# Kernel optimization log

Measured on AMD Instinct MI355X. Metric: run time of the kernel, lower is better.

The kernel has to match this reference:

```python
import jax, jax.numpy as jnp
import numpy as np
from jax import lax

N_HEAD, D_IN, D_HID, D_OUT = 8, 64, 64, 64
SEQ = 32768
STD = 1.0 / np.sqrt(D_HID * N_HEAD)


def _unif(key, shape):
    return jax.random.uniform(key, shape, jnp.float32, -STD, STD)


def setup_inputs() -> dict:
    key = jax.random.key(0)
    ks = jax.random.split(key, 12)
    D = N_HEAD * D_IN
    return {
        "inputs": jax.random.normal(ks[0], (SEQ, D), jnp.float32),
        "W_in": _unif(ks[1], (D, D)),
        "b_in": _unif(ks[2], (D,)),
        "W_gates": _unif(ks[3], (D_IN, 3 * D_HID)),
        "b_gates": _unif(ks[4], (3 * D_HID,)),
        "W_og": _unif(ks[5], (D_IN, D_HID)),
        "b_og": _unif(ks[6], (D_HID,)),
        "W_c": _unif(ks[7], (D_HID, D_OUT)),
        "b_c": _unif(ks[8], (D_OUT,)),
        "W_out": _unif(ks[9], (N_HEAD * D_OUT, N_HEAD * D_OUT)),
        "b_out": _unif(ks[10], (N_HEAD * D_OUT,)),
    }


def reference(inputs, W_in, b_in, W_gates, b_gates, W_og, b_og, W_c, b_c, W_out, b_out):
    S = inputs.shape[0]
    # input mixing across heads, then flatten: (S, H*d_in) -> (S*H, d_in)
    x = (inputs @ W_in + b_in).reshape(S * N_HEAD, D_IN)
    # FirstModule: fused gate projection
    g = x @ W_gates + b_gates  # (S*H, 3*d_hid)
    fg = jax.nn.sigmoid(g[:, :D_HID])
    ig = jax.nn.sigmoid(g[:, D_HID:2 * D_HID])
    h = jnp.tanh(g[:, 2 * D_HID:])
    hr = ig * h
    # linear recurrence c_t = fg_t * c_{t-1} + hr_t, c_0 = 0, via associative scan
    def comb(e1, e2):
        a1, b1 = e1
        a2, b2 = e2
        return (a1 * a2, b1 * a2 + b2)
    _, c = lax.associative_scan(comb, (fg, hr))  # (S*H, d_hid)
    # SecondModule: output gate and projection
    og = jax.nn.sigmoid(x @ W_og + b_og)
    o = (og * c) @ W_c + b_c  # (S*H, d_out)
    o = o.reshape(S, N_HEAD * D_OUT)
    return o @ W_out + b_out
```

## Files before the change

kernel.cpp:

```cpp
#include <hip/hip_runtime.h>


typedef unsigned short ushort;
typedef __bf16 bf16x8 __attribute__((ext_vector_type(8)));
typedef float f32x4 __attribute__((ext_vector_type(4)));

#define CROWS 64
#define NCH  4096
#define NSUP 64

#define GLOAD16(gp, lp) __builtin_amdgcn_global_load_lds( \
    (const __attribute__((address_space(1))) void*)(gp),  \
    (__attribute__((address_space(3))) void*)(lp), 16, 0, 0)

__device__ inline float b2f(ushort u) {
    return __builtin_bit_cast(float, (unsigned)u << 16);
}
__device__ inline ushort f2b(float f) {
    unsigned x = __builtin_bit_cast(unsigned, f);
    x += 0x7FFFu + ((x >> 16) & 1u);
    return (ushort)(x >> 16);
}
__device__ inline float sigm(float v) { return __builtin_amdgcn_rcpf(1.0f + __expf(-v)); }
__device__ inline float tanh_fast(float v) {
    return 2.0f * __builtin_amdgcn_rcpf(1.0f + __expf(-2.0f * v)) - 1.0f;
}
__device__ inline f32x4 MFMA(bf16x8 a, bf16x8 b, f32x4 c) {
    return __builtin_amdgcn_mfma_f32_16x16x32_bf16(a, b, c, 0, 0, 0);
}

__global__ void transpose512(const float* __restrict__ src, ushort* __restrict__ dst) {
    __shared__ float tile[32][33];
    const int tx = threadIdx.x & 31, ty = threadIdx.x >> 5;
    const int x0 = blockIdx.x * 32, y0 = blockIdx.y * 32;
    #pragma unroll
    for (int dy = 0; dy < 32; dy += 8)
        tile[ty + dy][tx] = src[(size_t)(y0 + ty + dy) * 512 + x0 + tx];
    __syncthreads();
    #pragma unroll
    for (int dy = 0; dy < 32; dy += 8)
        dst[(size_t)(x0 + ty + dy) * 512 + y0 + tx] = f2b(tile[tx][ty + dy]);
}

__global__ void prep_small(const float* __restrict__ W_gates, const float* __restrict__ W_og,
                           const float* __restrict__ W_c,
                           const float* __restrict__ b_gates, const float* __restrict__ b_og,
                           ushort* __restrict__ W2T, ushort* __restrict__ WcT, float* __restrict__ b2) {
    const int idx = blockIdx.x * 256 + threadIdx.x;
    if (idx < 16384) {
        const int n = idx >> 6, k = idx & 63;
        float v;
        if      (n < 64)  v = W_gates[k * 192 + 64 + n];
        else if (n < 128) v = W_gates[k * 192 + 128 + (n - 64)];
        else if (n < 192) v = W_gates[k * 192 + (n - 128)];
        else              v = W_og[k * 64 + (n - 192)];
        W2T[idx] = f2b(v);
    } else if (idx < 16384 + 4096) {
        const int i = idx - 16384;
        const int n = i >> 6, k = i & 63;
        WcT[i] = f2b(W_c[(k << 6) + n]);
    } else if (idx < 16384 + 4096 + 256) {
        const int i = idx - 20480;
        float v;
        if      (i < 64)  v = b_gates[64 + i];
        else if (i < 128) v = b_gates[128 + (i - 64)];
        else if (i < 192) v = b_gates[i - 128];
        else              v = b_og[i - 192];
        b2[i] = v;
    }
}

__global__ __launch_bounds__(256)
void cvt_f32_bf16(const float* __restrict__ src, ushort* __restrict__ dst) {
    const long i = ((long)blockIdx.x * 256 + threadIdx.x) * 8;
    const float4 v0 = *(const float4*)(src + i);
    const float4 v1 = *(const float4*)(src + i + 4);
    *(ushort4*)(dst + i)     = make_ushort4(f2b(v0.x), f2b(v0.y), f2b(v0.z), f2b(v0.w));
    *(ushort4*)(dst + i + 4) = make_ushort4(f2b(v1.x), f2b(v1.y), f2b(v1.z), f2b(v1.w));
}

template <int BM, int BN, int WAVES_M, int WAVES_N, int A32, int C32>
__global__ __launch_bounds__(256)
void gemm_bt(const void* __restrict__ Av, const ushort* __restrict__ Bt,
             const float* __restrict__ bias, void* __restrict__ Cv,
             int M, int N, int K) {
    constexpr int WM = BM / WAVES_M, WN = BN / WAVES_N;
    constexpr int MT = WM / 16, NT = WN / 16;
    __shared__ __align__(16) ushort sA[BM * 32];
    __shared__ __align__(16) ushort sB[BN * 32];

    const int t = threadIdx.x, w = t >> 6, lane = t & 63;
    const int wm = (w / WAVES_N) * WM, wn = (w % WAVES_N) * WN;
    const long bm = (long)blockIdx.x * BM, bn = (long)blockIdx.y * BN;

    f32x4 acc[MT][NT] = {};

    for (int k0 = 0; k0 < K; k0 += 32) {
        if (A32) {
            const float* A = (const float*)Av;
            #pragma unroll
            for (int is = 0; is < BM / 32; ++is) {
                const int row = is * 32 + (t >> 3);
                const int cd = (t & 7) >> 1, half = t & 1;
                const float4 v = *(const float4*)(A + (bm + row) * (long)K + k0 + (t & 7) * 4);
                *(ushort4*)&sA[row * 32 + ((cd ^ (row & 3)) * 8) + half * 4] =
                    make_ushort4(f2b(v.x), f2b(v.y), f2b(v.z), f2b(v.w));
            }
        } else {
            const ushort* A = (const ushort*)Av;
            #pragma unroll
            for (int is = 0; is < BM / 64; ++is) {
                const int row = t >> 2, kc = t & 3;
                GLOAD16(A + (bm + is * 64 + row) * (long)K + k0 + ((kc ^ (row & 3)) * 8),
                        (char*)sA + is * 4096 + w * 1024);
            }
        }
        #pragma unroll
        for (int is = 0; is < BN / 64; ++is) {
            const int row = t >> 2, kc = t & 3;
            GLOAD16(Bt + (bn + is * 64 + row) * (long)K + k0 + ((kc ^ (row & 3)) * 8),
                    (char*)sB + is * 4096 + w * 1024);
        }
        __syncthreads();

        bf16x8 af[MT], bfr[NT];
        #pragma unroll
        for (int i = 0; i < MT; ++i) {
            const int row = wm + i * 16 + (lane & 15), c = lane >> 4;
            af[i] = *(const bf16x8*)&sA[row * 32 + ((c ^ (row & 3)) * 8)];
        }
        #pragma unroll
        for (int j = 0; j < NT; ++j) {
            const int rb = wn + j * 16 + (lane & 15), c = lane >> 4;
            bfr[j] = *(const bf16x8*)&sB[rb * 32 + ((c ^ (rb & 3)) * 8)];
        }
        #pragma unroll
        for (int i = 0; i < MT; ++i)
            #pragma unroll
            for (int j = 0; j < NT; ++j)
                acc[i][j] = MFMA(af[i], bfr[j], acc[i][j]);
        __syncthreads();
    }

    #pragma unroll
    for (int i = 0; i < MT; ++i)
        #pragma unroll
        for (int j = 0; j < NT; ++j) {
            const long col = bn + wn + j * 16 + (lane & 15);
            const float bv = bias[col];
            #pragma unroll
            for (int r = 0; r < 4; ++r) {
                const long row = bm + wm + i * 16 + ((lane >> 4) << 2) + r;
                const float v = acc[i][j][r] + bv;
                if (C32) ((float*)Cv)[row * (long)N + col] = v;
                else     ((ushort*)Cv)[row * (long)N + col] = f2b(v);
            }
        }
}

template <int APPLY>
__global__ __launch_bounds__(256, 4)
void gates_scan(const ushort* __restrict__ X, const ushort* __restrict__ W2T,
                const float* __restrict__ b2, const ushort* __restrict__ WcT,
                const float* __restrict__ b_c,
                float* __restrict__ Agg, float* __restrict__ Bgg,
                const float* __restrict__ PreS, ushort* __restrict__ O) {
    __shared__ __align__(16) char smem[APPLY ? 35840 : 18432];
    ushort* sFG = (ushort*)smem;
    ushort* sHR = (ushort*)(smem + 9216);
    ushort* sOG = (ushort*)(smem + 18432);
    ushort* sP  = (ushort*)(smem + 27648);

    const int t = threadIdx.x, w = t >> 6, lane = t & 63;
    const int blk = blockIdx.x;
    const long row0 = (long)blk * CROWS;

    const int wm = (w >> 1) * 32;
    const int grpB = w & 1;
    const int colbase = grpB * 128;
    const int lr = lane & 15, lc = lane >> 4;

    bf16x8 af[2][2];
    #pragma unroll
    for (int kk = 0; kk < 2; ++kk)
        #pragma unroll
        for (int i = 0; i < 2; ++i)
            af[kk][i] = *(const bf16x8*)(X + (row0 + wm + i * 16 + lr) * 64 + kk * 32 + lc * 8);

    f32x4 acc[2][8] = {};
    #pragma unroll
    for (int kk = 0; kk < 2; ++kk)
        #pragma unroll
        for (int j = 0; j < 8; ++j) {
            const bf16x8 bf = *(const bf16x8*)(W2T + (colbase + j * 16 + lr) * 64 + kk * 32 + lc * 8);
            acc[0][j] = MFMA(af[kk][0], bf, acc[0][j]);
            acc[1][j] = MFMA(af[kk][1], bf, acc[1][j]);
        }

    if (!grpB) {
        #pragma unroll
        for (int jj = 0; jj < 4; ++jj) {
            const int ch = jj * 16 + lr;
            const float bi = b2[ch], bh = b2[64 + ch];
            #pragma unroll
            for (int i = 0; i < 2; ++i)
                #pragma unroll
                for (int r = 0; r < 4; ++r) {
                    const int row = wm + i * 16 + (lc << 2) + r;
                    const float gi = acc[i][jj][r] + bi;
                    const float gh = acc[i][jj + 4][r] + bh;
                    sHR[row * 72 + ch] = f2b(sigm(gi) * tanh_fast(gh));
                }
        }
    } else {
        #pragma unroll
        for (int jj = 0; jj < 4; ++jj) {
            const int ch = jj * 16 + lr;
            const float bfg = b2[128 + ch], bog = b2[192 + ch];
            #pragma unroll
            for (int i = 0; i < 2; ++i)
                #pragma unroll
                for (int r = 0; r < 4; ++r) {
                    const int row = wm + i * 16 + (lc << 2) + r;
                    sFG[row * 72 + ch] = f2b(sigm(acc[i][jj][r] + bfg));
                    if (APPLY) sOG[row * 72 + ch] = f2b(sigm(acc[i][jj + 4][r] + bog));
                }
        }
    }
    __syncthreads();

    if (!APPLY) {
        if (t < 64) {
            float a = 1.0f, b = 0.0f;
            #pragma unroll 8
            for (int r = 0; r < CROWS; ++r) {
                const float fg = b2f(sFG[r * 72 + t]);
                const float hr = b2f(sHR[r * 72 + t]);
                a *= fg;
                b = fmaf(b, fg, hr);
            }
            Agg[blk * 64 + t] = a;
            Bgg[blk * 64 + t] = b;
        }
        return;
    }

    if (t < 64) {
        float c = fmaf(PreS[(blk >> 6) * 64 + t], Agg[blk * 64 + t], Bgg[blk * 64 + t]);
        const int cch = t >> 3, half = t & 7;
        #pragma unroll 8
        for (int r = 0; r < CROWS; ++r) {
            const float fg = b2f(sFG[r * 72 + t]);
            const float hr = b2f(sHR[r * 72 + t]);
            c = fmaf(c, fg, hr);
            sP[r * 64 + ((cch ^ (r & 7)) * 8) + half] = f2b(b2f(sOG[r * 72 + t]) * c);
        }
    }
    __syncthreads();

    const int wn2 = grpB * 32;
    f32x4 acc2[2][2] = {};
    #pragma unroll
    for (int kk = 0; kk < 2; ++kk) {
        bf16x8 pa[2], wb[2];
        #pragma unroll
        for (int i = 0; i < 2; ++i) {
            const int row = wm + i * 16 + lr, c = kk * 4 + lc;
            pa[i] = *(const bf16x8*)&sP[row * 64 + ((c ^ (row & 7)) * 8)];
        }
        #pragma unroll
        for (int j = 0; j < 2; ++j)
            wb[j] = *(const bf16x8*)(WcT + (wn2 + j * 16 + lr) * 64 + kk * 32 + lc * 8);
        #pragma unroll
        for (int i = 0; i < 2; ++i)
            #pragma unroll
            for (int j = 0; j < 2; ++j)
                acc2[i][j] = MFMA(pa[i], wb[j], acc2[i][j]);
    }
    #pragma unroll
    for (int i = 0; i < 2; ++i)
        #pragma unroll
        for (int j = 0; j < 2; ++j) {
            const int col = wn2 + j * 16 + lr;
            const float bv = b_c[col];
            #pragma unroll
            for (int r = 0; r < 4; ++r) {
                const int row = wm + i * 16 + (lc << 2) + r;
                O[(row0 + row) * 64 + col] = f2b(acc2[i][j][r] + bv);
            }
        }
}

__global__ void scan_super(float* __restrict__ Agg, float* __restrict__ Bgg,
                           float* __restrict__ SA, float* __restrict__ SB) {
    const int s = blockIdx.x, ch = threadIdx.x;
    float a = 1.0f, b = 0.0f;
    #pragma unroll 8
    for (int j = 0; j < 64; ++j) {
        const int idx = (s * 64 + j) * 64 + ch;
        const float a2 = Agg[idx], bb = Bgg[idx];
        Agg[idx] = a;
        Bgg[idx] = b;
        a *= a2;
        b = fmaf(b, a2, bb);
    }
    SA[s * 64 + ch] = a;
    SB[s * 64 + ch] = b;
}

__global__ void scan_top(const float* __restrict__ SA, const float* __restrict__ SB,
                         float* __restrict__ PreS) {
    const int ch = threadIdx.x;
    float c = 0.0f;
    #pragma unroll 8
    for (int s = 0; s < 64; ++s) {
        PreS[s * 64 + ch] = c;
        c = fmaf(c, SA[s * 64 + ch], SB[s * 64 + ch]);
    }
}

extern "C" void kernel_launch(void* const* d_in, const int* in_sizes, int n_in,
                              void* d_out, int out_size, void* d_ws, size_t ws_size,
                              hipStream_t stream) {
    const float* inputs  = (const float*)d_in[0];
    const float* W_in    = (const float*)d_in[1];
    const float* b_in    = (const float*)d_in[2];
    const float* W_gates = (const float*)d_in[3];
    const float* b_gates = (const float*)d_in[4];
    const float* W_og    = (const float*)d_in[5];
    const float* b_og    = (const float*)d_in[6];
    const float* W_c     = (const float*)d_in[7];
    const float* b_c     = (const float*)d_in[8];
    const float* W_out   = (const float*)d_in[9];
    const float* b_out   = (const float*)d_in[10];
    float* out = (float*)d_out;

    char* ws = (char*)d_ws;
    ushort* X     = (ushort*)(ws);
    ushort* WinT  = (ushort*)(ws + 33554432);
    ushort* WoutT = (ushort*)(ws + 34078720);
    ushort* W2T   = (ushort*)(ws + 34603008);
    ushort* WcT   = (ushort*)(ws + 34635776);
    float*  b2    = (float*)(ws + 34643968);
    float*  Agg   = (float*)(ws + 34644992);
    float*  Bgg   = (float*)(ws + 35693568);
    float*  SA    = (float*)(ws + 36742144);
    float*  SB    = (float*)(ws + 36758528);
    float*  PreS  = (float*)(ws + 36774912);
    ushort* Ibf   = (ushort*)(ws + 36791296);
    ushort* O = X;
    const bool big_ws = ws_size >= (36791296ull + 33554432ull);

    transpose512<<<dim3(16, 16), 256, 0, stream>>>(W_in, WinT);
    transpose512<<<dim3(16, 16), 256, 0, stream>>>(W_out, WoutT);
    prep_small<<<81, 256, 0, stream>>>(W_gates, W_og, W_c, b_gates, b_og, W2T, WcT, b2);

    if (big_ws) {
        cvt_f32_bf16<<<8192, 256, 0, stream>>>(inputs, Ibf);
        gemm_bt<128, 128, 2, 2, 0, 0><<<dim3(256, 4), 256, 0, stream>>>(
            Ibf, WinT, b_in, X, 32768, 512, 512);
    } else {
        gemm_bt<128, 128, 2, 2, 1, 0><<<dim3(256, 4), 256, 0, stream>>>(
            inputs, WinT, b_in, X, 32768, 512, 512);
    }

    gates_scan<0><<<NCH, 256, 0, stream>>>(X, W2T, b2, WcT, b_c, Agg, Bgg, PreS, O);
    scan_super<<<NSUP, 64, 0, stream>>>(Agg, Bgg, SA, SB);
    scan_top<<<1, 64, 0, stream>>>(SA, SB, PreS);
    gates_scan<1><<<NCH, 256, 0, stream>>>(X, W2T, b2, WcT, b_c, Agg, Bgg, PreS, O);

    gemm_bt<128, 128, 2, 2, 0, 1><<<dim3(256, 4), 256, 0, stream>>>(
        O, WoutT, b_out, out, 32768, 512, 512);
}
```

Before: 317.2 us.

## Store gate activations in first pass to avoid recomputing GEMM in apply pass

Adds a gates_store kernel that computes the gate projection once, writes packed bf16 forget/hr pairs and the output gate to global memory, and emits per-chunk scan aggregates. A new scan_apply kernel rereads those stored values instead of reloading X and recomputing the gate MFMA and transcendentals, then applies the prefix and the W_c projection. This trades recomputation for extra global traffic (about 12 bytes per element written and read back) and uses d_out as scratch for the output gate. The new path runs only when the workspace is large enough.

New measurement: 288.6 us. -9.0%, faster.

```diff
diff --git a/kernel.cpp b/kernel.cpp
--- a/kernel.cpp
+++ b/kernel.cpp
@@ -158,6 +158,192 @@
         }
 }
 
+__global__ __launch_bounds__(256, 4)
+void gates_store(const ushort* __restrict__ X, const ushort* __restrict__ W2T,
+                 const float* __restrict__ b2,
+                 unsigned* __restrict__ FGHR, ushort* __restrict__ OGg,
+                 float* __restrict__ Agg, float* __restrict__ Bgg) {
+    __shared__ __align__(16) char smem[29696];
+    ushort* sFG = (ushort*)smem;
+    ushort* sHR = (ushort*)(smem + 9216);
+    ushort* sOG = (ushort*)(smem + 18432);
+    float*  spa = (float*)(smem + 27648);
+    float*  spb = (float*)(smem + 28672);
+
+    const int t = threadIdx.x, w = t >> 6, lane = t & 63;
+    const int blk = blockIdx.x;
+    const long row0 = (long)blk * CROWS;
+
+    const int wm = (w >> 1) * 32;
+    const int grpB = w & 1;
+    const int colbase = grpB * 128;
+    const int lr = lane & 15, lc = lane >> 4;
+
+    bf16x8 af[2][2];
+    #pragma unroll
+    for (int kk = 0; kk < 2; ++kk)
+        #pragma unroll
+        for (int i = 0; i < 2; ++i)
+            af[kk][i] = *(const bf16x8*)(X + (row0 + wm + i * 16 + lr) * 64 + kk * 32 + lc * 8);
+
+    f32x4 acc[2][8] = {};
+    #pragma unroll
+    for (int kk = 0; kk < 2; ++kk)
+        #pragma unroll
+        for (int j = 0; j < 8; ++j) {
+            const bf16x8 bf = *(const bf16x8*)(W2T + (colbase + j * 16 + lr) * 64 + kk * 32 + lc * 8);
+            acc[0][j] = MFMA(af[kk][0], bf, acc[0][j]);
+            acc[1][j] = MFMA(af[kk][1], bf, acc[1][j]);
+        }
+
+    if (!grpB) {
+        #pragma unroll
+        for (int jj = 0; jj < 4; ++jj) {
+            const int ch = jj * 16 + lr;
+            const float bi = b2[ch], bh = b2[64 + ch];
+            #pragma unroll
+            for (int i = 0; i < 2; ++i)
+                #pragma unroll
+                for (int r = 0; r < 4; ++r) {
+                    const int row = wm + i * 16 + (lc << 2) + r;
+                    const float gi = acc[i][jj][r] + bi;
+                    const float gh = acc[i][jj + 4][r] + bh;
+                    sHR[row * 72 + ch] = f2b(sigm(gi) * tanh_fast(gh));
+                }
+        }
+    } else {
+        #pragma unroll
+        for (int jj = 0; jj < 4; ++jj) {
+            const int ch = jj * 16 + lr;
+            const float bfg = b2[128 + ch], bog = b2[192 + ch];
+            #pragma unroll
+            for (int i = 0; i < 2; ++i)
+                #pragma unroll
+                for (int r = 0; r < 4; ++r) {
+                    const int row = wm + i * 16 + (lc << 2) + r;
+                    sFG[row * 72 + ch] = f2b(sigm(acc[i][jj][r] + bfg));
+                    sOG[row * 72 + ch] = f2b(sigm(acc[i][jj + 4][r] + bog));
+                }
+        }
+    }
+    __syncthreads();
+
+    {
+        const int ch = lane;
+        float a = 1.0f, b = 0.0f;
+        #pragma unroll
+        for (int r = 0; r < 16; ++r) {
+            const int row = (w << 4) + r;
+            const ushort ufg = sFG[row * 72 + ch];
+            const ushort uhr = sHR[row * 72 + ch];
+            FGHR[(row0 + row) * 64 + ch] = (unsigned)ufg | ((unsigned)uhr << 16);
+            OGg[(row0 + row) * 64 + ch] = sOG[row * 72 + ch];
+            const float fg = b2f(ufg), hr = b2f(uhr);
+            a *= fg;
+            b = fmaf(b, fg, hr);
+        }
+        spa[(w << 6) + ch] = a;
+        spb[(w << 6) + ch] = b;
+    }
+    __syncthreads();
+
+    if (t < 64) {
+        float a = spa[t], b = spb[t];
+        #pragma unroll
+        for (int k = 1; k < 4; ++k) {
+            const float a2 = spa[(k << 6) + t];
+            const float bb = spb[(k << 6) + t];
+            a *= a2;
+            b = fmaf(b, a2, bb);
+        }
+        Agg[blk * 64 + t] = a;
+        Bgg[blk * 64 + t] = b;
+    }
+}
+
+__global__ __launch_bounds__(256, 4)
+void scan_apply(const unsigned* __restrict__ FGHR, const ushort* __restrict__ OGg,
+                const float* __restrict__ Agg, const float* __restrict__ Bgg,
+                const float* __restrict__ PreS,
+                const ushort* __restrict__ WcT, const float* __restrict__ b_c,
+                ushort* __restrict__ O) {
+    __shared__ __align__(16) char smem[10240];
+    ushort* sP  = (ushort*)smem;
+    float*  spa = (float*)(smem + 8192);
+    float*  spb = (float*)(smem + 9216);
+
+    const int t = threadIdx.x, w = t >> 6, lane = t & 63;
+    const int blk = blockIdx.x;
+    const long row0 = (long)blk * CROWS;
+    const int ch = lane;
+
+    unsigned fh[16];
+    {
+        float a = 1.0f, b = 0.0f;
+        #pragma unroll
+        for (int r = 0; r < 16; ++r) {
+            fh[r] = FGHR[(row0 + (w << 4) + r) * 64 + ch];
+            const float fg = b2f((ushort)fh[r]);
+            const float hr = b2f((ushort)(fh[r] >> 16));
+            a *= fg;
+            b = fmaf(b, fg, hr);
+        }
+        spa[(w << 6) + ch] = a;
+        spb[(w << 6) + ch] = b;
+    }
+    __syncthreads();
+
+    float c = fmaf(PreS[(blk >> 6) * 64 + ch], Agg[blk * 64 + ch], Bgg[blk * 64 + ch]);
+    for (int k = 0; k < w; ++k)
+        c = fmaf(c, spa[(k << 6) + ch], spb[(k << 6) + ch]);
+
+    const int cch = ch >> 3, half = ch & 7;
+    #pragma unroll
+    for (int r = 0; r < 16; ++r) {
+        const int row = (w << 4) + r;
+        const float fg = b2f((ushort)fh[r]);
+        const float hr = b2f((ushort)(fh[r] >> 16));
+        c = fmaf(c, fg, hr);
+        const float og = b2f(OGg[(row0 + row) * 64 + ch]);
+        sP[row * 64 + ((cch ^ (row & 7)) * 8) + half] = f2b(og * c);
+    }
+    __syncthreads();
+
+    const int wm = (w >> 1) * 32;
+    const int wn2 = (w & 1) * 32;
+    const int lr = lane & 15, lc = lane >> 4;
+    f32x4 acc2[2][2] = {};
+    #pragma unroll
+    for (int kk = 0; kk < 2; ++kk) {
+        bf16x8 pa[2], wb[2];
+        #pragma unroll
+        for (int i = 0; i < 2; ++i) {
+            const int row = wm + i * 16 + lr, cidx = kk * 4 + lc;
+            pa[i] = *(const bf16x8*)&sP[row * 64 + ((cidx ^ (row & 7)) * 8)];
+        }
+        #pragma unroll
+        for (int j = 0; j < 2; ++j)
+            wb[j] = *(const bf16x8*)(WcT + (wn2 + j * 16 + lr) * 64 + kk * 32 + lc * 8);
+        #pragma unroll
+        for (int i = 0; i < 2; ++i)
+            #pragma unroll
+            for (int j = 0; j < 2; ++j)
+                acc2[i][j] = MFMA(pa[i], wb[j], acc2[i][j]);
+    }
+    #pragma unroll
+    for (int i = 0; i < 2; ++i)
+        #pragma unroll
+        for (int j = 0; j < 2; ++j) {
+            const int col = wn2 + j * 16 + lr;
+            const float bv = b_c[col];
+            #pragma unroll
+            for (int r = 0; r < 4; ++r) {
+                const int row = wm + i * 16 + (lc << 2) + r;
+                O[(row0 + row) * 64 + col] = f2b(acc2[i][j][r] + bv);
+            }
+        }
+}
+
 template <int APPLY>
 __global__ __launch_bounds__(256, 4)
 void gates_scan(const ushort* __restrict__ X, const ushort* __restrict__ W2T,
@@ -348,26 +534,41 @@
     float*  SB    = (float*)(ws + 36758528);
     float*  PreS  = (float*)(ws + 36774912);
     ushort* Ibf   = (ushort*)(ws + 36791296);
+    unsigned* FGHR = (unsigned*)(ws + 36791296);
+    ushort* OGg   = (ushort*)d_out;
     ushort* O = X;
-    const bool big_ws = ws_size >= (36791296ull + 33554432ull);
+
+    const bool new_path = ws_size >= 103900160ull;
+    const bool big_ws   = ws_size >= 70345728ull;
 
     transpose512<<<dim3(16, 16), 256, 0, stream>>>(W_in, WinT);
     transpose512<<<dim3(16, 16), 256, 0, stream>>>(W_out, WoutT);
     prep_small<<<81, 256, 0, stream>>>(W_gates, W_og, W_c, b_gates, b_og, W2T, WcT, b2);
 
-    if (big_ws) {
+    if (new_path) {
         cvt_f32_bf16<<<8192, 256, 0, stream>>>(inputs, Ibf);
         gemm_bt<128, 128, 2, 2, 0, 0><<<dim3(256, 4), 256, 0, stream>>>(
             Ibf, WinT, b_in, X, 32768, 512, 512);
+        gates_store<<<NCH, 256, 0, stream>>>(X, W2T, b2, FGHR, OGg, Agg, Bgg);
+        scan_super<<<NSUP, 64, 0, stream>>>(Agg, Bgg, SA, SB);
+        scan_top<<<1, 64, 0, stream>>>(SA, SB, PreS);
+        scan_apply<<<NCH, 256, 0, stream>>>(FGHR, OGg, Agg, Bgg, PreS, WcT, b_c, O);
+    } else if (big_ws) {
+        cvt_f32_bf16<<<8192, 256, 0, stream>>>(inputs, Ibf);
+        gemm_bt<128, 128, 2, 2, 0, 0><<<dim3(256, 4), 256, 0, stream>>>(
+            Ibf, WinT, b_in, X, 32768, 512, 512);
+        gates_scan<0><<<NCH, 256, 0, stream>>>(X, W2T, b2, WcT, b_c, Agg, Bgg, PreS, O);
+        scan_super<<<NSUP, 64, 0, stream>>>(Agg, Bgg, SA, SB);
+        scan_top<<<1, 64, 0, stream>>>(SA, SB, PreS);
+        gates_scan<1><<<NCH, 256, 0, stream>>>(X, W2T, b2, WcT, b_c, Agg, Bgg, PreS, O);
     } else {
         gemm_bt<128, 128, 2, 2, 1, 0><<<dim3(256, 4), 256, 0, stream>>>(
             inputs, WinT, b_in, X, 32768, 512, 512);
-    }
-
-    gates_scan<0><<<NCH, 256, 0, stream>>>(X, W2T, b2, WcT, b_c, Agg, Bgg, PreS, O);
-    scan_super<<<NSUP, 64, 0, stream>>>(Agg, Bgg, SA, SB);
-    scan_top<<<1, 64, 0, stream>>>(SA, SB, PreS);
-    gates_scan<1><<<NCH, 256, 0, stream>>>(X, W2T, b2, WcT, b_c, Agg, Bgg, PreS, O);
+        gates_scan<0><<<NCH, 256, 0, stream>>>(X, W2T, b2, WcT, b_c, Agg, Bgg, PreS, O);
+        scan_super<<<NSUP, 64, 0, stream>>>(Agg, Bgg, SA, SB);
+        scan_top<<<1, 64, 0, stream>>>(SA, SB, PreS);
+        gates_scan<1><<<NCH, 256, 0, stream>>>(X, W2T, b2, WcT, b_c, Agg, Bgg, PreS, O);
+    }
 
     gemm_bt<128, 128, 2, 2, 0, 1><<<dim3(256, 4), 256, 0, stream>>>(
         O, WoutT, b_out, out, 32768, 512, 512);
```

## Give each wavefront its own 64-row chunk in gate/scan kernels

Applied to the files above, without the earlier changes.

Adds gates_agg and scan_apply kernels, used on the large-workspace path, in which each wavefront owns a whole 64-row chunk. It computes gate projections with MFMA in 16-row sub-tiles, stages packed forget/input values in per-wave LDS and runs the per-channel recurrence with all 64 lanes, one channel per lane. The old kernels left three of four waves idle during the serial scan and synchronised the whole block. The new layout drops block-wide barriers and makes all lanes scan, at the cost of reloading weights from global memory per wave and using smaller MFMA tiles. The Wc projection is folded into the same per-wave loop.

New measurement: 348.4 us. 1.1x slower.

```diff
diff --git a/kernel.cpp b/kernel.cpp
--- a/kernel.cpp
+++ b/kernel.cpp
@@ -158,6 +158,148 @@
         }
 }
 
+__global__ __launch_bounds__(256, 4)
+void gates_agg(const ushort* __restrict__ X, const ushort* __restrict__ W2T,
+               const float* __restrict__ b2,
+               float* __restrict__ Agg, float* __restrict__ Bgg) {
+    __shared__ __align__(16) unsigned sW[4][16 * 64];
+
+    const int t = threadIdx.x, w = t >> 6, lane = t & 63;
+    const int lr = lane & 15, lc = lane >> 4;
+    const long chunk = (long)blockIdx.x * 4 + w;
+    const long row0 = chunk * 64;
+
+    float a = 1.0f, b = 0.0f;
+    #pragma unroll 1
+    for (int bt = 0; bt < 4; ++bt) {
+        const long rb = row0 + bt * 16;
+        const bf16x8 af0 = *(const bf16x8*)(X + (rb + lr) * 64 + lc * 8);
+        const bf16x8 af1 = *(const bf16x8*)(X + (rb + lr) * 64 + 32 + lc * 8);
+
+        #pragma unroll
+        for (int g = 0; g < 4; ++g) {
+            f32x4 aig = {}, ah = {}, afg = {};
+            #pragma unroll
+            for (int kk = 0; kk < 2; ++kk) {
+                const bf16x8 w0 = *(const bf16x8*)(W2T + (g * 16 + lr) * 64 + kk * 32 + lc * 8);
+                const bf16x8 w1 = *(const bf16x8*)(W2T + (64 + g * 16 + lr) * 64 + kk * 32 + lc * 8);
+                const bf16x8 w2 = *(const bf16x8*)(W2T + (128 + g * 16 + lr) * 64 + kk * 32 + lc * 8);
+                const bf16x8 afk = kk ? af1 : af0;
+                aig = MFMA(afk, w0, aig);
+                ah  = MFMA(afk, w1, ah);
+                afg = MFMA(afk, w2, afg);
+            }
+            const int ch = g * 16 + lr;
+            const float bi = b2[ch], bh = b2[64 + ch], bfg = b2[128 + ch];
+            #pragma unroll
+            for (int r = 0; r < 4; ++r) {
+                const int row = (lc << 2) + r;
+                const float hr = sigm(aig[r] + bi) * tanh_fast(ah[r] + bh);
+                const float fg = sigm(afg[r] + bfg);
+                sW[w][row * 64 + (ch ^ (lc << 4))] =
+                    (unsigned)f2b(fg) | ((unsigned)f2b(hr) << 16);
+            }
+        }
+        #pragma unroll
+        for (int r = 0; r < 16; ++r) {
+            const unsigned fh = sW[w][r * 64 + (lane ^ ((r >> 2) << 4))];
+            const float fg = b2f((ushort)fh);
+            const float hr = b2f((ushort)(fh >> 16));
+            a *= fg;
+            b = fmaf(b, fg, hr);
+        }
+    }
+    Agg[chunk * 64 + lane] = a;
+    Bgg[chunk * 64 + lane] = b;
+}
+
+__global__ __launch_bounds__(256, 4)
+void scan_apply(const ushort* __restrict__ X, const ushort* __restrict__ W2T,
+                const float* __restrict__ b2,
+                const float* __restrict__ Agg, const float* __restrict__ Bgg,
+                const float* __restrict__ PreS,
+                const ushort* __restrict__ WcT, const float* __restrict__ b_c,
+                ushort* __restrict__ O) {
+    __shared__ __align__(16) unsigned sW[4][16 * 64];
+    __shared__ __align__(16) ushort  sOG[4][16 * 64];
+    __shared__ __align__(16) ushort  sP [4][16 * 64];
+
+    const int t = threadIdx.x, w = t >> 6, lane = t & 63;
+    const int lr = lane & 15, lc = lane >> 4;
+    const long chunk = (long)blockIdx.x * 4 + w;
+    const long row0 = chunk * 64;
+
+    float c = fmaf(PreS[(chunk >> 6) * 64 + lane], Agg[chunk * 64 + lane],
+                   Bgg[chunk * 64 + lane]);
+
+    const int cch = lane >> 3, half = lane & 7;
+
+    #pragma unroll 1
+    for (int bt = 0; bt < 4; ++bt) {
+        const long rb = row0 + bt * 16;
+        const bf16x8 af0 = *(const bf16x8*)(X + (rb + lr) * 64 + lc * 8);
+        const bf16x8 af1 = *(const bf16x8*)(X + (rb + lr) * 64 + 32 + lc * 8);
+
+        #pragma unroll
+        for (int g = 0; g < 4; ++g) {
+            f32x4 aig = {}, ah = {}, afg = {}, aog = {};
+            #pragma unroll
+            for (int kk = 0; kk < 2; ++kk) {
+                const bf16x8 w0 = *(const bf16x8*)(W2T + (g * 16 + lr) * 64 + kk * 32 + lc * 8);
+                const bf16x8 w1 = *(const bf16x8*)(W2T + (64 + g * 16 + lr) * 64 + kk * 32 + lc * 8);
+                const bf16x8 w2 = *(const bf16x8*)(W2T + (128 + g * 16 + lr) * 64 + kk * 32 + lc * 8);
+                const bf16x8 w3 = *(const bf16x8*)(W2T + (192 + g * 16 + lr) * 64 + kk * 32 + lc * 8);
+                const bf16x8 afk = kk ? af1 : af0;
+                aig = MFMA(afk, w0, aig);
+                ah  = MFMA(afk, w1, ah);
+                afg = MFMA(afk, w2, afg);
+                aog = MFMA(afk, w3, aog);
+            }
+            const int ch = g * 16 + lr;
+            const float bi = b2[ch], bh = b2[64 + ch];
+            const float bfg = b2[128 + ch], bog = b2[192 + ch];
+            #pragma unroll
+            for (int r = 0; r < 4; ++r) {
+                const int row = (lc << 2) + r;
+                const float hr = sigm(aig[r] + bi) * tanh_fast(ah[r] + bh);
+                const float fg = sigm(afg[r] + bfg);
+                const int sl = row * 64 + (ch ^ (lc << 4));
+                sW[w][sl]  = (unsigned)f2b(fg) | ((unsigned)f2b(hr) << 16);
+                sOG[w][sl] = f2b(sigm(aog[r] + bog));
+            }
+        }
+
+        #pragma unroll
+        for (int r = 0; r < 16; ++r) {
+            const int sl = r * 64 + (lane ^ ((r >> 2) << 4));
+            const unsigned fh = sW[w][sl];
+            const float og = b2f(sOG[w][sl]);
+            c = fmaf(c, b2f((ushort)fh), b2f((ushort)(fh >> 16)));
+            sP[w][r * 64 + ((cch ^ (r & 7)) * 8) + half] = f2b(og * c);
+        }
+
+        f32x4 acc2[4] = {};
+        #pragma unroll
+        for (int kk = 0; kk < 2; ++kk) {
+            const int cidx = kk * 4 + lc;
+            const bf16x8 pa = *(const bf16x8*)&sP[w][lr * 64 + ((cidx ^ (lr & 7)) * 8)];
+            #pragma unroll
+            for (int j = 0; j < 4; ++j) {
+                const bf16x8 wc = *(const bf16x8*)(WcT + (j * 16 + lr) * 64 + kk * 32 + lc * 8);
+                acc2[j] = MFMA(pa, wc, acc2[j]);
+            }
+        }
+        #pragma unroll
+        for (int j = 0; j < 4; ++j) {
+            const int col = j * 16 + lr;
+            const float bv = b_c[col];
+            #pragma unroll
+            for (int r = 0; r < 4; ++r)
+                O[(rb + (lc << 2) + r) * 64 + col] = f2b(acc2[j][r] + bv);
+        }
+    }
+}
+
 template <int APPLY>
 __global__ __launch_bounds__(256, 4)
 void gates_scan(const ushort* __restrict__ X, const ushort* __restrict__ W2T,
@@ -262,7 +404,7 @@
     f32x4 acc2[2][2] = {};
     #pragma unroll
     for (int kk = 0; kk < 2; ++kk) {
-        bf16x8 pa[2], wb[2];
+        bf16x8 pa[2], wbx[2];
         #pragma unroll
         for (int i = 0; i < 2; ++i) {
             const int row = wm + i * 16 + lr, c = kk * 4 + lc;
@@ -270,12 +412,12 @@
         }
         #pragma unroll
         for (int j = 0; j < 2; ++j)
-            wb[j] = *(const bf16x8*)(WcT + (wn2 + j * 16 + lr) * 64 + kk * 32 + lc * 8);
+            wbx[j] = *(const bf16x8*)(WcT + (wn2 + j * 16 + lr) * 64 + kk * 32 + lc * 8);
         #pragma unroll
         for (int i = 0; i < 2; ++i)
             #pragma unroll
             for (int j = 0; j < 2; ++j)
-                acc2[i][j] = MFMA(pa[i], wb[j], acc2[i][j]);
+                acc2[i][j] = MFMA(pa[i], wbx[j], acc2[i][j]);
     }
     #pragma unroll
     for (int i = 0; i < 2; ++i)
@@ -349,7 +491,8 @@
     float*  PreS  = (float*)(ws + 36774912);
     ushort* Ibf   = (ushort*)(ws + 36791296);
     ushort* O = X;
-    const bool big_ws = ws_size >= (36791296ull + 33554432ull);
+
+    const bool big_ws = ws_size >= 70345728ull;
 
     transpose512<<<dim3(16, 16), 256, 0, stream>>>(W_in, WinT);
     transpose512<<<dim3(16, 16), 256, 0, stream>>>(W_out, WoutT);
@@ -359,15 +502,18 @@
         cvt_f32_bf16<<<8192, 256, 0, stream>>>(inputs, Ibf);
         gemm_bt<128, 128, 2, 2, 0, 0><<<dim3(256, 4), 256, 0, stream>>>(
             Ibf, WinT, b_in, X, 32768, 512, 512);
+        gates_agg<<<NCH / 4, 256, 0, stream>>>(X, W2T, b2, Agg, Bgg);
+        scan_super<<<NSUP, 64, 0, stream>>>(Agg, Bgg, SA, SB);
+        scan_top<<<1, 64, 0, stream>>>(SA, SB, PreS);
+        scan_apply<<<NCH / 4, 256, 0, stream>>>(X, W2T, b2, Agg, Bgg, PreS, WcT, b_c, O);
     } else {
         gemm_bt<128, 128, 2, 2, 1, 0><<<dim3(256, 4), 256, 0, stream>>>(
             inputs, WinT, b_in, X, 32768, 512, 512);
-    }
-
-    gates_scan<0><<<NCH, 256, 0, stream>>>(X, W2T, b2, WcT, b_c, Agg, Bgg, PreS, O);
-    scan_super<<<NSUP, 64, 0, stream>>>(Agg, Bgg, SA, SB);
-    scan_top<<<1, 64, 0, stream>>>(SA, SB, PreS);
-    gates_scan<1><<<NCH, 256, 0, stream>>>(X, W2T, b2, WcT, b_c, Agg, Bgg, PreS, O);
+        gates_scan<0><<<NCH, 256, 0, stream>>>(X, W2T, b2, WcT, b_c, Agg, Bgg, PreS, O);
+        scan_super<<<NSUP, 64, 0, stream>>>(Agg, Bgg, SA, SB);
+        scan_top<<<1, 64, 0, stream>>>(SA, SB, PreS);
+        gates_scan<1><<<NCH, 256, 0, stream>>>(X, W2T, b2, WcT, b_c, Agg, Bgg, PreS, O);
+    }
 
     gemm_bt<128, 128, 2, 2, 0, 1><<<dim3(256, 4), 256, 0, stream>>>(
         O, WoutT, b_out, out, 32768, 512, 512);
```
